# Performance work log

Hardware: AMD Instinct MI355X
Metric: run time of the kernel (lower is better)

The kernel has to match this reference:

```python
import jax, jax.numpy as jnp
import numpy as np

B, S, D = 2, 2048, 2048
H, KV, HD = 16, 8, 128
THETA = 1000000.0
EPS = 1e-6


def rms_norm(x, w, eps=EPS):
    # normalize over last dim (head_dim), per Qwen3 q_norm/k_norm
    var = jnp.mean(jnp.square(x), axis=-1, keepdims=True)
    return x * jax.lax.rsqrt(var + eps) * w


def rope_cos_sin(seq_len, head_dim, theta=THETA, dtype=jnp.float32):
    inv_freq = 1.0 / (theta ** (jnp.arange(0, head_dim, 2, dtype=jnp.float32) / head_dim))
    pos = jnp.arange(seq_len, dtype=jnp.float32)
    freqs = jnp.outer(pos, inv_freq)              # [S, HD/2]
    emb = jnp.concatenate([freqs, freqs], axis=-1)  # [S, HD]
    return jnp.cos(emb).astype(dtype), jnp.sin(emb).astype(dtype)


def rotate_half(x):
    x1, x2 = jnp.split(x, 2, axis=-1)
    return jnp.concatenate([-x2, x1], axis=-1)


def setup_inputs() -> dict:
    key = jax.random.key(0)
    ks = jax.random.split(key, 8)
    sd = 1.0 / np.sqrt(D)
    return {
        "x": jax.random.normal(ks[0], (B, S, D), jnp.float32),
        "attention_mask": jnp.zeros((B, 1, S, S), jnp.float32),
        "wq": jax.random.normal(ks[1], (H * HD, D), jnp.float32) * sd,
        "wk": jax.random.normal(ks[2], (KV * HD, D), jnp.float32) * sd,
        "wv": jax.random.normal(ks[3], (KV * HD, D), jnp.float32) * sd,
        "wo": jax.random.normal(ks[4], (D, H * HD), jnp.float32) * sd,
        "q_norm_w": jnp.ones((HD,), jnp.float32),
        "k_norm_w": jnp.ones((HD,), jnp.float32),
    }


def reference(x, attention_mask, wq, wk, wv, wo, q_norm_w, k_norm_w):
    b, s, d = x.shape
    # QKV projections
    q = (x @ wq.T).reshape(b, s, H, HD)
    k = (x @ wk.T).reshape(b, s, KV, HD)
    v = (x @ wv.T).reshape(b, s, KV, HD)
    # Qwen3 per-head RMSNorm on q and k
    q = rms_norm(q, q_norm_w)
    k = rms_norm(k, k_norm_w)
    # RoPE
    cos, sin = rope_cos_sin(s, HD, dtype=x.dtype)
    cos = cos[None, :, None, :]
    sin = sin[None, :, None, :]
    q = q * cos + rotate_half(q) * sin
    k = k * cos + rotate_half(k) * sin
    # GQA: repeat kv heads to H query heads
    rep = H // KV
    k = jnp.repeat(k, rep, axis=2)  # [b, s, H, HD]
    v = jnp.repeat(v, rep, axis=2)
    # attention
    scale = 1.0 / np.sqrt(HD)
    logits = jnp.einsum("bqhd,bkhd->bhqk", q, k) * scale
    logits = logits + attention_mask
    causal = jnp.tril(jnp.ones((s, s), bool))
    logits = jnp.where(causal[None, None], logits, jnp.asarray(-1e9, logits.dtype))
    probs = jax.nn.softmax(logits, axis=-1)
    out = jnp.einsum("bhqk,bkhd->bqhd", probs, v).reshape(b, s, H * HD)
    return out @ wo.T
```

## Files before the change

kernel.cpp:

```cpp
#include <hip/hip_runtime.h>
#include <hip/hip_bf16.h>

typedef unsigned short u16;
typedef __attribute__((ext_vector_type(8))) short s16x8;
typedef __attribute__((ext_vector_type(4))) float f32x4;

#define NB 2
#define SQ 2048
#define DM 2048
#define NH 16
#define NKV 8
#define HD 128

__device__ __forceinline__ float bf2f(u16 u) {
    return __uint_as_float(((unsigned)u) << 16);
}
__device__ __forceinline__ u16 f2bf(float f) {
    unsigned u = __float_as_uint(f);
    u += 0x7FFFu + ((u >> 16) & 1u);
    return (u16)(u >> 16);
}

__device__ __forceinline__ void gload16(const void* g, void* l) {
    __builtin_amdgcn_global_load_lds((__attribute__((address_space(1))) void*)g,
                                     (__attribute__((address_space(3))) void*)l,
                                     16, 0, 0);
}

#define X4   2097152u
#define WQ4  1048576u
#define WK4   524288u
#define WV4   524288u
#define WO4  1048576u
#define P0 X4
#define P1 (P0 + WQ4)
#define P2 (P1 + WK4)
#define P3 (P2 + WV4)
#define P4 (P3 + WO4)

__global__ __launch_bounds__(256) void cvt5(const float* __restrict__ x,
                                            const float* __restrict__ wq,
                                            const float* __restrict__ wk,
                                            const float* __restrict__ wv,
                                            const float* __restrict__ wo,
                                            u16* __restrict__ xb, u16* __restrict__ wqb,
                                            u16* __restrict__ wkb, u16* __restrict__ wvb,
                                            u16* __restrict__ wob) {
    unsigned i4 = blockIdx.x * 256u + threadIdx.x;
    if (i4 >= P4) return;
    const float* src; u16* dst; unsigned off;
    if (i4 < P0)      { src = x;  dst = xb;  off = i4; }
    else if (i4 < P1) { src = wq; dst = wqb; off = i4 - P0; }
    else if (i4 < P2) { src = wk; dst = wkb; off = i4 - P1; }
    else if (i4 < P3) { src = wv; dst = wvb; off = i4 - P2; }
    else              { src = wo; dst = wob; off = i4 - P3; }
    float4 v = ((const float4*)src)[off];
    ushort4 o;
    o.x = f2bf(v.x); o.y = f2bf(v.y); o.z = f2bf(v.z); o.w = f2bf(v.w);
    ((ushort4*)dst)[off] = o;
}

__global__ __launch_bounds__(512) void gemm_qkv(const u16* __restrict__ A,
                                                const u16* __restrict__ wqb,
                                                const u16* __restrict__ wkb,
                                                const u16* __restrict__ wvb,
                                                u16* __restrict__ q_ws,
                                                u16* __restrict__ k_ws,
                                                u16* __restrict__ vt_ws) {
    __shared__ u16 SA[2][2][256 * 32];
    __shared__ u16 SB[2][2][256 * 32];
    const int K = DM;
    const int t_ = threadIdx.x;
    const int w = t_ >> 6, lane = t_ & 63;
    const int lr = lane & 15, lg = lane >> 4;
    const int bid = blockIdx.x;
    const int swz = (bid & 7) * 32 + (bid >> 3);
    const int m0 = (swz >> 4) * 256, n0 = (swz & 15) * 256;
    const int wr = w >> 2, wc = w & 3;

    const u16* W; int nloc;
    if (n0 < 2048)      { W = wqb; nloc = n0; }
    else if (n0 < 3072) { W = wkb; nloc = n0 - 2048; }
    else                { W = wvb; nloc = n0 - 3072; }

    const int srow = t_ >> 2;
    const int sc4 = t_ & 3;
    const int schk = (sc4 ^ ((srow >> 1) & 3)) * 8;

#define STG_A(ks, bufq, kk)                                                      \
    {                                                                            \
        gload16(&A[(size_t)(m0 + srow) * K + (kk) + (ks)*32 + schk],             \
                &SA[bufq][ks][(w * 16) * 32]);                                   \
        gload16(&A[(size_t)(m0 + 128 + srow) * K + (kk) + (ks)*32 + schk],       \
                &SA[bufq][ks][(128 + w * 16) * 32]);                             \
    }
#define STG_B(ks, bufq, kk)                                                      \
    {                                                                            \
        gload16(&W[(size_t)(nloc + srow) * K + (kk) + (ks)*32 + schk],           \
                &SB[bufq][ks][(w * 16) * 32]);                                   \
        gload16(&W[(size_t)(nloc + 128 + srow) * K + (kk) + (ks)*32 + schk],     \
                &SB[bufq][ks][(128 + w * 16) * 32]);                             \
    }

    f32x4 acc[8][4];
#pragma unroll
    for (int i = 0; i < 8; ++i)
#pragma unroll
        for (int j = 0; j < 4; ++j) acc[i][j] = (f32x4){0.f, 0.f, 0.f, 0.f};

    const int rchk = (lg ^ ((lr >> 1) & 3)) * 8;

    STG_A(0, 0, 0); STG_B(0, 0, 0); STG_A(1, 0, 0); STG_B(1, 0, 0);
    asm volatile("s_waitcnt vmcnt(4)\n\ts_barrier" ::: "memory");

    const int NT = K / 64;
    for (int t = 0; t < NT; ++t) {
        const int pb = t & 1, nbuf = pb ^ 1;
        const int kk = (t + 1) * 64;
        const bool more = (t < NT - 1);

        s16x8 af[4], bf[4];

        if (more) STG_A(0, nbuf, kk);
#pragma unroll
        for (int fc = 0; fc < 4; ++fc)
            bf[fc] = *(const s16x8*)&SB[pb][0][(wc * 64 + fc * 16 + lr) * 32 + rchk];
#pragma unroll
        for (int fi = 0; fi < 4; ++fi)
            af[fi] = *(const s16x8*)&SA[pb][0][(wr * 128 + fi * 16 + lr) * 32 + rchk];
        __builtin_amdgcn_s_setprio(1);
#pragma unroll
        for (int fi = 0; fi < 4; ++fi)
#pragma unroll
            for (int fc = 0; fc < 4; ++fc)
                acc[fi][fc] = __builtin_amdgcn_mfma_f32_16x16x32_bf16(
                    af[fi], bf[fc], acc[fi][fc], 0, 0, 0);
        __builtin_amdgcn_s_setprio(0);

        if (more) STG_B(0, nbuf, kk);
#pragma unroll
        for (int fi = 0; fi < 4; ++fi)
            af[fi] = *(const s16x8*)&SA[pb][0][(wr * 128 + 64 + fi * 16 + lr) * 32 + rchk];
        __builtin_amdgcn_s_setprio(1);
#pragma unroll
        for (int fi = 0; fi < 4; ++fi)
#pragma unroll
            for (int fc = 0; fc < 4; ++fc)
                acc[4 + fi][fc] = __builtin_amdgcn_mfma_f32_16x16x32_bf16(
                    af[fi], bf[fc], acc[4 + fi][fc], 0, 0, 0);
        __builtin_amdgcn_s_setprio(0);

        if (more) asm volatile("s_waitcnt vmcnt(4)\n\ts_barrier" ::: "memory");
        else      asm volatile("s_waitcnt vmcnt(0)\n\ts_barrier" ::: "memory");

        if (more) STG_A(1, nbuf, kk);
#pragma unroll
        for (int fc = 0; fc < 4; ++fc)
            bf[fc] = *(const s16x8*)&SB[pb][1][(wc * 64 + fc * 16 + lr) * 32 + rchk];
#pragma unroll
        for (int fi = 0; fi < 4; ++fi)
            af[fi] = *(const s16x8*)&SA[pb][1][(wr * 128 + fi * 16 + lr) * 32 + rchk];
        __builtin_amdgcn_s_setprio(1);
#pragma unroll
        for (int fi = 0; fi < 4; ++fi)
#pragma unroll
            for (int fc = 0; fc < 4; ++fc)
                acc[fi][fc] = __builtin_amdgcn_mfma_f32_16x16x32_bf16(
                    af[fi], bf[fc], acc[fi][fc], 0, 0, 0);
        __builtin_amdgcn_s_setprio(0);

        if (more) STG_B(1, nbuf, kk);
#pragma unroll
        for (int fi = 0; fi < 4; ++fi)
            af[fi] = *(const s16x8*)&SA[pb][1][(wr * 128 + 64 + fi * 16 + lr) * 32 + rchk];
        __builtin_amdgcn_s_setprio(1);
#pragma unroll
        for (int fi = 0; fi < 4; ++fi)
#pragma unroll
            for (int fc = 0; fc < 4; ++fc)
                acc[4 + fi][fc] = __builtin_amdgcn_mfma_f32_16x16x32_bf16(
                    af[fi], bf[fc], acc[4 + fi][fc], 0, 0, 0);
        __builtin_amdgcn_s_setprio(0);

        if (more) asm volatile("s_waitcnt vmcnt(4)\n\ts_barrier" ::: "memory");
    }
#undef STG_A
#undef STG_B

#pragma unroll
    for (int fr = 0; fr < 8; ++fr)
#pragma unroll
        for (int fc = 0; fc < 4; ++fc)
#pragma unroll
            for (int j = 0; j < 4; ++j) {
                int m = m0 + wr * 128 + fr * 16 + lg * 4 + j;
                int n = n0 + wc * 64 + fc * 16 + lr;
                u16 v = f2bf(acc[fr][fc][j]);
                if (n0 < 2048) {
                    q_ws[(size_t)m * 2048 + n] = v;
                } else if (n0 < 3072) {
                    k_ws[(size_t)m * 1024 + (n - 2048)] = v;
                } else {
                    int b = m >> 11, sl = m & 2047;
                    vt_ws[((size_t)b * 1024 + (n - 3072)) * 2048 + sl] = v;
                }
            }
}

__global__ __launch_bounds__(256) void gemm_out(const u16* __restrict__ A,
                                                const u16* __restrict__ W,
                                                float* __restrict__ C,
                                                int M, int N, int K) {
    __shared__ u16 Alds[128 * 32];
    __shared__ u16 Blds[128 * 32];
    const int t = threadIdx.x;
    const int w = t >> 6, lane = t & 63;
    const int lr = lane & 15, lg = lane >> 4;
    const int m0 = blockIdx.y * 128, n0 = blockIdx.x * 128;
    const int wr = w >> 1, wc = w & 1;

    f32x4 acc[4][4];
#pragma unroll
    for (int i = 0; i < 4; ++i)
#pragma unroll
        for (int j = 0; j < 4; ++j) acc[i][j] = (f32x4){0.f, 0.f, 0.f, 0.f};

    const int r_a = lane >> 2;
    const int c_a = (lane & 3) * 8;

    for (int k0 = 0; k0 < K; k0 += 32) {
#pragma unroll
        for (int s = 0; s < 2; ++s) {
            int chunk = s * 4 + w;
            int row = chunk * 16 + r_a;
            gload16(&A[(size_t)(m0 + row) * K + k0 + c_a], &Alds[chunk * 512]);
            gload16(&W[(size_t)(n0 + row) * K + k0 + c_a], &Blds[chunk * 512]);
        }
        asm volatile("s_waitcnt vmcnt(0)" ::: "memory");
        __syncthreads();

        s16x8 af[4], bfr[4];
#pragma unroll
        for (int mi = 0; mi < 4; ++mi)
            af[mi] = *(const s16x8*)&Alds[(wr * 64 + mi * 16 + lr) * 32 + lg * 8];
#pragma unroll
        for (int ni = 0; ni < 4; ++ni)
            bfr[ni] = *(const s16x8*)&Blds[(wc * 64 + ni * 16 + lr) * 32 + lg * 8];
#pragma unroll
        for (int mi = 0; mi < 4; ++mi)
#pragma unroll
            for (int ni = 0; ni < 4; ++ni)
                acc[mi][ni] = __builtin_amdgcn_mfma_f32_16x16x32_bf16(
                    af[mi], bfr[ni], acc[mi][ni], 0, 0, 0);
        __syncthreads();
    }

#pragma unroll
    for (int mi = 0; mi < 4; ++mi)
#pragma unroll
        for (int ni = 0; ni < 4; ++ni)
#pragma unroll
            for (int j = 0; j < 4; ++j) {
                int m = m0 + wr * 64 + mi * 16 + lg * 4 + j;
                int n = n0 + wc * 64 + ni * 16 + lr;
                C[(size_t)m * N + n] = acc[mi][ni][j];
            }
}

__global__ __launch_bounds__(256) void rmsrope(u16* __restrict__ qb, u16* __restrict__ kb,
                                               const float* __restrict__ qw,
                                               const float* __restrict__ kw) {
    int wid = blockIdx.x * 4 + (threadIdx.x >> 6);
    int lane = threadIdx.x & 63;
    u16* base;
    const float* w;
    int pos;
    float sc;
    if (wid < NB * SQ * NH) {
        int h = wid & (NH - 1), tok = wid >> 4;
        pos = tok & (SQ - 1);
        base = qb + ((size_t)tok * NH + h) * HD;
        w = qw;
        sc = 0.08838834764831845f;
    } else {
        int f = wid - NB * SQ * NH;
        int h = f & (NKV - 1), tok = f >> 3;
        pos = tok & (SQ - 1);
        base = kb + ((size_t)tok * NKV + h) * HD;
        w = kw;
        sc = 1.0f;
    }
    float x1 = bf2f(base[lane]), x2 = bf2f(base[lane + 64]);
    float ss = x1 * x1 + x2 * x2;
#pragma unroll
    for (int off = 32; off; off >>= 1) ss += __shfl_xor(ss, off);
    float r = rsqrtf(ss * (1.f / 128.f) + 1e-6f);
    x1 *= r * w[lane];
    x2 *= r * w[lane + 64];
    float inv = exp2f((float)lane * (-19.931568569324174f / 64.f));
    float fr = (float)pos * inv;
    float c = cosf(fr);
    float sn = sinf(fr);
    base[lane]      = f2bf(sc * (x1 * c - x2 * sn));
    base[lane + 64] = f2bf(sc * (x2 * c + x1 * sn));
}

__global__ __launch_bounds__(256) void flash(const u16* __restrict__ q,
                                             const u16* __restrict__ k,
                                             const u16* __restrict__ vt,
                                             u16* __restrict__ o) {
    __shared__ u16 KB[64][128];
    __shared__ u16 VB[128][64];
    __shared__ u16 plds[4][16][72];
    const int id = blockIdx.x;
    const int i_ = id >> 3;
    const int g = (id & 7) * 2 + (i_ >> 5);
    const int kvh = g >> 1, b = g & 1;
    const int j_ = i_ & 31;
    const int h = kvh * 2 + (j_ >> 4);
    const int bx = j_ & 15;
    const int t = threadIdx.x;
    const int w = t >> 6, lane = t & 63;
    const int lr = lane & 15, lg = lane >> 4;

    const u16* kbase = k + (size_t)(b * SQ) * 1024 + kvh * 128;
    const u16* vbase = vt + (size_t)(b * NKV + kvh) * HD * SQ;

    for (int sidx = 0; sidx < 2; ++sidx) {
        const int qt = sidx ? (31 - bx) : bx;
        const int qrow = qt * 64 + w * 16;

        s16x8 qf[4];
        const size_t qbase = ((size_t)(b * SQ + qrow + lr) * NH + h) * HD;
#pragma unroll
        for (int ds = 0; ds < 4; ++ds)
            qf[ds] = *(const s16x8*)&q[qbase + ds * 32 + lg * 8];

        f32x4 oacc[8];
#pragma unroll
        for (int dt = 0; dt < 8; ++dt) oacc[dt] = (f32x4){0.f, 0.f, 0.f, 0.f};
        float mrow[4] = {-1e30f, -1e30f, -1e30f, -1e30f};
        float lrow[4] = {0.f, 0.f, 0.f, 0.f};

#pragma unroll
        for (int i = 0; i < 4; ++i) {
            int qq = i * 256 + t;
            int r = qq >> 4, c = qq & 15;
            gload16(kbase + (size_t)r * 1024 + (c ^ (r & 7)) * 8,
                    &KB[0][0] + i * 2048 + w * 512);
        }
        __syncthreads();

        for (int kt = 0; kt <= qt; ++kt) {
            const int kv0 = kt * 64;
#pragma unroll
            for (int i = 0; i < 4; ++i) {
                int qq = i * 256 + t;
                int r = qq >> 3, c = qq & 7;
                gload16(vbase + (size_t)r * SQ + kv0 + (c ^ (r & 7)) * 8,
                        &VB[0][0] + i * 2048 + w * 512);
            }

            f32x4 sc[4];
#pragma unroll
            for (int ct = 0; ct < 4; ++ct) sc[ct] = (f32x4){0.f, 0.f, 0.f, 0.f};
#pragma unroll
            for (int ds = 0; ds < 4; ++ds) {
                s16x8 kf[4];
#pragma unroll
                for (int ct = 0; ct < 4; ++ct)
                    kf[ct] = *(const s16x8*)&KB[ct * 16 + lr][((ds * 4 + lg) ^ (lr & 7)) * 8];
                __builtin_amdgcn_s_setprio(1);
#pragma unroll
                for (int ct = 0; ct < 4; ++ct)
                    sc[ct] = __builtin_amdgcn_mfma_f32_16x16x32_bf16(qf[ds], kf[ct], sc[ct], 0, 0, 0);
                __builtin_amdgcn_s_setprio(0);
            }
            if (kt == qt) {
#pragma unroll
                for (int ct = 0; ct < 4; ++ct)
#pragma unroll
                    for (int j = 0; j < 4; ++j)
                        if ((kv0 + ct * 16 + lr) > (qrow + lg * 4 + j))
                            sc[ct][j] = -1e30f;
            }
            float mnew[4], sfac[4];
#pragma unroll
            for (int j = 0; j < 4; ++j) {
                float tm = fmaxf(fmaxf(sc[0][j], sc[1][j]), fmaxf(sc[2][j], sc[3][j]));
#pragma unroll
                for (int off = 1; off < 16; off <<= 1) tm = fmaxf(tm, __shfl_xor(tm, off));
                mnew[j] = fmaxf(mrow[j], tm);
                sfac[j] = __expf(mrow[j] - mnew[j]);
                mrow[j] = mnew[j];
            }
#pragma unroll
            for (int ct = 0; ct < 4; ++ct)
#pragma unroll
                for (int j = 0; j < 4; ++j) sc[ct][j] = __expf(sc[ct][j] - mnew[j]);
#pragma unroll
            for (int j = 0; j < 4; ++j) {
                float ssum = sc[0][j] + sc[1][j] + sc[2][j] + sc[3][j];
#pragma unroll
                for (int off = 1; off < 16; off <<= 1) ssum += __shfl_xor(ssum, off);
                lrow[j] = lrow[j] * sfac[j] + ssum;
            }
#pragma unroll
            for (int dt = 0; dt < 8; ++dt)
#pragma unroll
                for (int j = 0; j < 4; ++j) oacc[dt][j] *= sfac[j];

#pragma unroll
            for (int ct = 0; ct < 4; ++ct)
#pragma unroll
                for (int j = 0; j < 4; ++j)
                    plds[w][lg * 4 + j][ct * 16 + lr] = f2bf(sc[ct][j]);
            s16x8 pf0 = *(const s16x8*)&plds[w][lr][lg * 8];
            s16x8 pf1 = *(const s16x8*)&plds[w][lr][32 + lg * 8];

            __syncthreads();

            if (kt < qt) {
#pragma unroll
                for (int i = 0; i < 4; ++i) {
                    int qq = i * 256 + t;
                    int r = qq >> 4, c = qq & 15;
                    gload16(kbase + (size_t)(kv0 + 64 + r) * 1024 + (c ^ (r & 7)) * 8,
                            &KB[0][0] + i * 2048 + w * 512);
                }
            }

#pragma unroll
            for (int dt = 0; dt < 8; ++dt) {
                s16x8 vf0 = *(const s16x8*)&VB[dt * 16 + lr][(lg ^ (lr & 7)) * 8];
                s16x8 vf1 = *(const s16x8*)&VB[dt * 16 + lr][((4 + lg) ^ (lr & 7)) * 8];
                __builtin_amdgcn_s_setprio(1);
                oacc[dt] = __builtin_amdgcn_mfma_f32_16x16x32_bf16(pf0, vf0, oacc[dt], 0, 0, 0);
                oacc[dt] = __builtin_amdgcn_mfma_f32_16x16x32_bf16(pf1, vf1, oacc[dt], 0, 0, 0);
                __builtin_amdgcn_s_setprio(0);
            }
            __syncthreads();
        }

        float inv_l[4];
#pragma unroll
        for (int j = 0; j < 4; ++j) inv_l[j] = 1.f / lrow[j];
#pragma unroll
        for (int dt = 0; dt < 8; ++dt)
#pragma unroll
            for (int j = 0; j < 4; ++j) {
                int tok = b * SQ + qrow + lg * 4 + j;
                o[((size_t)tok * NH + h) * HD + dt * 16 + lr] = f2bf(oacc[dt][j] * inv_l[j]);
            }
    }
}

extern "C" void kernel_launch(void* const* d_in, const int* in_sizes, int n_in,
                              void* d_out, int out_size, void* d_ws, size_t ws_size,
                              hipStream_t stream) {
    (void)in_sizes; (void)n_in; (void)out_size; (void)ws_size;
    const float* x   = (const float*)d_in[0];
    const float* wq  = (const float*)d_in[2];
    const float* wk  = (const float*)d_in[3];
    const float* wv  = (const float*)d_in[4];
    const float* wo  = (const float*)d_in[5];
    const float* qnw = (const float*)d_in[6];
    const float* knw = (const float*)d_in[7];

    u16* xb    = (u16*)d_ws;
    u16* q_ws  = xb    + (size_t)4096 * 2048;
    u16* k_ws  = q_ws  + (size_t)4096 * 2048;
    u16* vt_ws = k_ws  + (size_t)4096 * 1024;
    u16* wqb   = vt_ws + (size_t)4096 * 1024;
    u16* wkb   = wqb   + (size_t)2048 * 2048;
    u16* wvb   = wkb   + (size_t)1024 * 2048;
    u16* wob   = wvb   + (size_t)1024 * 2048;

    const int M = NB * SQ;

    cvt5<<<(P4 + 255) / 256, 256, 0, stream>>>(x, wq, wk, wv, wo, xb, wqb, wkb, wvb, wob);

    gemm_qkv<<<256, 512, 0, stream>>>(xb, wqb, wkb, wvb, q_ws, k_ws, vt_ws);

    rmsrope<<<(NB * SQ * (NH + NKV)) / 4, 256, 0, stream>>>(q_ws, k_ws, qnw, knw);

    flash<<<512, 256, 0, stream>>>(q_ws, k_ws, vt_ws, q_ws);

    gemm_out<<<dim3(DM / 128, M / 128), 256, 0, stream>>>(q_ws, wob, (float*)d_out, M, DM, DM);
}
```

Before: 279.9 us.

## Use three-stage LDS ring buffer with one barrier per k-slice in QKV GEMM

The QKV projection GEMM moves from a double-buffered pair of 64-wide k-tiles to a three-slot ring of 32-wide k-slices. Each iteration waits on one barrier and prefetches two slices ahead. This cuts LDS use from 64KB to 48KB and keeps more loads in flight. In exchange it doubles the number of loop iterations and barriers per k extent, and the per-barrier MFMA work is smaller.

Measured after the change: 286.4 us. +2.3%, slower.

```diff
diff --git a/kernel.cpp b/kernel.cpp
--- a/kernel.cpp
+++ b/kernel.cpp
@@ -67,8 +67,8 @@
                                                 u16* __restrict__ q_ws,
                                                 u16* __restrict__ k_ws,
                                                 u16* __restrict__ vt_ws) {
-    __shared__ u16 SA[2][2][256 * 32];
-    __shared__ u16 SB[2][2][256 * 32];
+    __shared__ u16 SA[3][256 * 32];
+    __shared__ u16 SB[3][256 * 32];
     const int K = DM;
     const int t_ = threadIdx.x;
     const int w = t_ >> 6, lane = t_ & 63;
@@ -87,20 +87,19 @@
     const int sc4 = t_ & 3;
     const int schk = (sc4 ^ ((srow >> 1) & 3)) * 8;
 
-#define STG_A(ks, bufq, kk)                                                      \
+#define STG(tt)                                                                  \
     {                                                                            \
-        gload16(&A[(size_t)(m0 + srow) * K + (kk) + (ks)*32 + schk],             \
-                &SA[bufq][ks][(w * 16) * 32]);                                   \
-        gload16(&A[(size_t)(m0 + 128 + srow) * K + (kk) + (ks)*32 + schk],       \
-                &SA[bufq][ks][(128 + w * 16) * 32]);                             \
+        const int kb_ = (tt) * 32;                                               \
+        const int bq_ = (tt) % 3;                                                \
+        gload16(&A[(size_t)(m0 + srow) * K + kb_ + schk],                        \
+                &SA[bq_][(w * 16) * 32]);                                        \
+        gload16(&A[(size_t)(m0 + 128 + srow) * K + kb_ + schk],                  \
+                &SA[bq_][(128 + w * 16) * 32]);                                  \
+        gload16(&W[(size_t)(nloc + srow) * K + kb_ + schk],                      \
+                &SB[bq_][(w * 16) * 32]);                                        \
+        gload16(&W[(size_t)(nloc + 128 + srow) * K + kb_ + schk],                \
+                &SB[bq_][(128 + w * 16) * 32]);                                  \
     }
-#define STG_B(ks, bufq, kk)                                                      \
-    {                                                                            \
-        gload16(&W[(size_t)(nloc + srow) * K + (kk) + (ks)*32 + schk],           \
-                &SB[bufq][ks][(w * 16) * 32]);                                   \
-        gload16(&W[(size_t)(nloc + 128 + srow) * K + (kk) + (ks)*32 + schk],     \
-                &SB[bufq][ks][(128 + w * 16) * 32]);                             \
-    }
 
     f32x4 acc[8][4];
 #pragma unroll
@@ -110,24 +109,24 @@
 
     const int rchk = (lg ^ ((lr >> 1) & 3)) * 8;
 
-    STG_A(0, 0, 0); STG_B(0, 0, 0); STG_A(1, 0, 0); STG_B(1, 0, 0);
-    asm volatile("s_waitcnt vmcnt(4)\n\ts_barrier" ::: "memory");
-
-    const int NT = K / 64;
+    STG(0); STG(1);
+
+    const int NT = K / 32;
     for (int t = 0; t < NT; ++t) {
-        const int pb = t & 1, nbuf = pb ^ 1;
-        const int kk = (t + 1) * 64;
-        const bool more = (t < NT - 1);
-
+        if (t < NT - 1) asm volatile("s_waitcnt vmcnt(4)\n\ts_barrier" ::: "memory");
+        else            asm volatile("s_waitcnt vmcnt(0)\n\ts_barrier" ::: "memory");
+        if (t + 2 < NT) STG(t + 2);
+
+        const u16* pA = &SA[t % 3][0];
+        const u16* pB = &SB[t % 3][0];
         s16x8 af[4], bf[4];
-
-        if (more) STG_A(0, nbuf, kk);
 #pragma unroll
         for (int fc = 0; fc < 4; ++fc)
-            bf[fc] = *(const s16x8*)&SB[pb][0][(wc * 64 + fc * 16 + lr) * 32 + rchk];
+            bf[fc] = *(const s16x8*)&pB[(wc * 64 + fc * 16 + lr) * 32 + rchk];
+
 #pragma unroll
         for (int fi = 0; fi < 4; ++fi)
-            af[fi] = *(const s16x8*)&SA[pb][0][(wr * 128 + fi * 16 + lr) * 32 + rchk];
+            af[fi] = *(const s16x8*)&pA[(wr * 128 + fi * 16 + lr) * 32 + rchk];
         __builtin_amdgcn_s_setprio(1);
 #pragma unroll
         for (int fi = 0; fi < 4; ++fi)
@@ -137,10 +136,9 @@
                     af[fi], bf[fc], acc[fi][fc], 0, 0, 0);
         __builtin_amdgcn_s_setprio(0);
 
-        if (more) STG_B(0, nbuf, kk);
 #pragma unroll
         for (int fi = 0; fi < 4; ++fi)
-            af[fi] = *(const s16x8*)&SA[pb][0][(wr * 128 + 64 + fi * 16 + lr) * 32 + rchk];
+            af[fi] = *(const s16x8*)&pA[(wr * 128 + 64 + fi * 16 + lr) * 32 + rchk];
         __builtin_amdgcn_s_setprio(1);
 #pragma unroll
         for (int fi = 0; fi < 4; ++fi)
@@ -149,43 +147,8 @@
                 acc[4 + fi][fc] = __builtin_amdgcn_mfma_f32_16x16x32_bf16(
                     af[fi], bf[fc], acc[4 + fi][fc], 0, 0, 0);
         __builtin_amdgcn_s_setprio(0);
-
-        if (more) asm volatile("s_waitcnt vmcnt(4)\n\ts_barrier" ::: "memory");
-        else      asm volatile("s_waitcnt vmcnt(0)\n\ts_barrier" ::: "memory");
-
-        if (more) STG_A(1, nbuf, kk);
-#pragma unroll
-        for (int fc = 0; fc < 4; ++fc)
-            bf[fc] = *(const s16x8*)&SB[pb][1][(wc * 64 + fc * 16 + lr) * 32 + rchk];
-#pragma unroll
-        for (int fi = 0; fi < 4; ++fi)
-            af[fi] = *(const s16x8*)&SA[pb][1][(wr * 128 + fi * 16 + lr) * 32 + rchk];
-        __builtin_amdgcn_s_setprio(1);
-#pragma unroll
-        for (int fi = 0; fi < 4; ++fi)
-#pragma unroll
-            for (int fc = 0; fc < 4; ++fc)
-                acc[fi][fc] = __builtin_amdgcn_mfma_f32_16x16x32_bf16(
-                    af[fi], bf[fc], acc[fi][fc], 0, 0, 0);
-        __builtin_amdgcn_s_setprio(0);
-
-        if (more) STG_B(1, nbuf, kk);
-#pragma unroll
-        for (int fi = 0; fi < 4; ++fi)
-            af[fi] = *(const s16x8*)&SA[pb][1][(wr * 128 + 64 + fi * 16 + lr) * 32 + rchk];
-        __builtin_amdgcn_s_setprio(1);
-#pragma unroll
-        for (int fi = 0; fi < 4; ++fi)
-#pragma unroll
-            for (int fc = 0; fc < 4; ++fc)
-                acc[4 + fi][fc] = __builtin_amdgcn_mfma_f32_16x16x32_bf16(
-                    af[fi], bf[fc], acc[4 + fi][fc], 0, 0, 0);
-        __builtin_amdgcn_s_setprio(0);
-
-        if (more) asm volatile("s_waitcnt vmcnt(4)\n\ts_barrier" ::: "memory");
     }
-#undef STG_A
-#undef STG_B
+#undef STG
 
 #pragma unroll
     for (int fr = 0; fr < 8; ++fr)
```

## Rewrite output GEMM with 256x256 tiles, double-buffered LDS, swizzle

Applied to the files above, without the earlier changes.

Replaces the simple 128x128 output-projection GEMM with a 512-thread 256x256-tile kernel. It double-buffers 64-wide K slices in LDS and overlaps the next tile's global-to-LDS loads with MFMA work. It also XOR-swizzles LDS chunks to reduce bank conflicts, remaps block indices for L2 locality, and raises wave priority around the MFMA bursts. Only 128 blocks launch, which may leave some of the chip's many CUs idle, and the larger register and LDS footprint lowers occupancy.

Result: slower. 290.8 us (+3.9%).

```diff
diff --git a/kernel.cpp b/kernel.cpp
--- a/kernel.cpp
+++ b/kernel.cpp
@@ -207,63 +207,133 @@
             }
 }
 
-__global__ __launch_bounds__(256) void gemm_out(const u16* __restrict__ A,
+__global__ __launch_bounds__(512) void gemm_out(const u16* __restrict__ A,
                                                 const u16* __restrict__ W,
-                                                float* __restrict__ C,
-                                                int M, int N, int K) {
-    __shared__ u16 Alds[128 * 32];
-    __shared__ u16 Blds[128 * 32];
-    const int t = threadIdx.x;
-    const int w = t >> 6, lane = t & 63;
+                                                float* __restrict__ C) {
+    __shared__ u16 SA[2][2][256 * 32];
+    __shared__ u16 SB[2][2][256 * 32];
+    const int K = DM;
+    const int t_ = threadIdx.x;
+    const int w = t_ >> 6, lane = t_ & 63;
     const int lr = lane & 15, lg = lane >> 4;
-    const int m0 = blockIdx.y * 128, n0 = blockIdx.x * 128;
-    const int wr = w >> 1, wc = w & 1;
-
-    f32x4 acc[4][4];
-#pragma unroll
-    for (int i = 0; i < 4; ++i)
+    const int bid = blockIdx.x;
+    const int swz = (bid & 7) * 16 + (bid >> 3);
+    const int m0 = (swz >> 3) * 256, n0 = (swz & 7) * 256;
+    const int wr = w >> 2, wc = w & 3;
+
+    const int srow = t_ >> 2;
+    const int sc4 = t_ & 3;
+    const int schk = (sc4 ^ ((srow >> 1) & 3)) * 8;
+
+#define STG_A(ks, bufq, kk)                                                      \
+    {                                                                            \
+        gload16(&A[(size_t)(m0 + srow) * K + (kk) + (ks)*32 + schk],             \
+                &SA[bufq][ks][(w * 16) * 32]);                                   \
+        gload16(&A[(size_t)(m0 + 128 + srow) * K + (kk) + (ks)*32 + schk],       \
+                &SA[bufq][ks][(128 + w * 16) * 32]);                             \
+    }
+#define STG_B(ks, bufq, kk)                                                      \
+    {                                                                            \
+        gload16(&W[(size_t)(n0 + srow) * K + (kk) + (ks)*32 + schk],             \
+                &SB[bufq][ks][(w * 16) * 32]);                                   \
+        gload16(&W[(size_t)(n0 + 128 + srow) * K + (kk) + (ks)*32 + schk],       \
+                &SB[bufq][ks][(128 + w * 16) * 32]);                             \
+    }
+
+    f32x4 acc[8][4];
+#pragma unroll
+    for (int i = 0; i < 8; ++i)
 #pragma unroll
         for (int j = 0; j < 4; ++j) acc[i][j] = (f32x4){0.f, 0.f, 0.f, 0.f};
 
-    const int r_a = lane >> 2;
-    const int c_a = (lane & 3) * 8;
-
-    for (int k0 = 0; k0 < K; k0 += 32) {
-#pragma unroll
-        for (int s = 0; s < 2; ++s) {
-            int chunk = s * 4 + w;
-            int row = chunk * 16 + r_a;
-            gload16(&A[(size_t)(m0 + row) * K + k0 + c_a], &Alds[chunk * 512]);
-            gload16(&W[(size_t)(n0 + row) * K + k0 + c_a], &Blds[chunk * 512]);
-        }
-        asm volatile("s_waitcnt vmcnt(0)" ::: "memory");
-        __syncthreads();
-
-        s16x8 af[4], bfr[4];
-#pragma unroll
-        for (int mi = 0; mi < 4; ++mi)
-            af[mi] = *(const s16x8*)&Alds[(wr * 64 + mi * 16 + lr) * 32 + lg * 8];
-#pragma unroll
-        for (int ni = 0; ni < 4; ++ni)
-            bfr[ni] = *(const s16x8*)&Blds[(wc * 64 + ni * 16 + lr) * 32 + lg * 8];
-#pragma unroll
-        for (int mi = 0; mi < 4; ++mi)
-#pragma unroll
-            for (int ni = 0; ni < 4; ++ni)
-                acc[mi][ni] = __builtin_amdgcn_mfma_f32_16x16x32_bf16(
-                    af[mi], bfr[ni], acc[mi][ni], 0, 0, 0);
-        __syncthreads();
-    }
-
-#pragma unroll
-    for (int mi = 0; mi < 4; ++mi)
-#pragma unroll
-        for (int ni = 0; ni < 4; ++ni)
+    const int rchk = (lg ^ ((lr >> 1) & 3)) * 8;
+
+    STG_A(0, 0, 0); STG_B(0, 0, 0); STG_A(1, 0, 0); STG_B(1, 0, 0);
+    asm volatile("s_waitcnt vmcnt(4)\n\ts_barrier" ::: "memory");
+
+    const int NT = K / 64;
+    for (int t = 0; t < NT; ++t) {
+        const int pb = t & 1, nbuf = pb ^ 1;
+        const int kk = (t + 1) * 64;
+        const bool more = (t < NT - 1);
+
+        s16x8 af[4], bf[4];
+
+        if (more) STG_A(0, nbuf, kk);
+#pragma unroll
+        for (int fc = 0; fc < 4; ++fc)
+            bf[fc] = *(const s16x8*)&SB[pb][0][(wc * 64 + fc * 16 + lr) * 32 + rchk];
+#pragma unroll
+        for (int fi = 0; fi < 4; ++fi)
+            af[fi] = *(const s16x8*)&SA[pb][0][(wr * 128 + fi * 16 + lr) * 32 + rchk];
+        __builtin_amdgcn_s_setprio(1);
+#pragma unroll
+        for (int fi = 0; fi < 4; ++fi)
+#pragma unroll
+            for (int fc = 0; fc < 4; ++fc)
+                acc[fi][fc] = __builtin_amdgcn_mfma_f32_16x16x32_bf16(
+                    af[fi], bf[fc], acc[fi][fc], 0, 0, 0);
+        __builtin_amdgcn_s_setprio(0);
+
+        if (more) STG_B(0, nbuf, kk);
+#pragma unroll
+        for (int fi = 0; fi < 4; ++fi)
+            af[fi] = *(const s16x8*)&SA[pb][0][(wr * 128 + 64 + fi * 16 + lr) * 32 + rchk];
+        __builtin_amdgcn_s_setprio(1);
+#pragma unroll
+        for (int fi = 0; fi < 4; ++fi)
+#pragma unroll
+            for (int fc = 0; fc < 4; ++fc)
+                acc[4 + fi][fc] = __builtin_amdgcn_mfma_f32_16x16x32_bf16(
+                    af[fi], bf[fc], acc[4 + fi][fc], 0, 0, 0);
+        __builtin_amdgcn_s_setprio(0);
+
+        if (more) asm volatile("s_waitcnt vmcnt(4)\n\ts_barrier" ::: "memory");
+        else      asm volatile("s_waitcnt vmcnt(0)\n\ts_barrier" ::: "memory");
+
+        if (more) STG_A(1, nbuf, kk);
+#pragma unroll
+        for (int fc = 0; fc < 4; ++fc)
+            bf[fc] = *(const s16x8*)&SB[pb][1][(wc * 64 + fc * 16 + lr) * 32 + rchk];
+#pragma unroll
+        for (int fi = 0; fi < 4; ++fi)
+            af[fi] = *(const s16x8*)&SA[pb][1][(wr * 128 + fi * 16 + lr) * 32 + rchk];
+        __builtin_amdgcn_s_setprio(1);
+#pragma unroll
+        for (int fi = 0; fi < 4; ++fi)
+#pragma unroll
+            for (int fc = 0; fc < 4; ++fc)
+                acc[fi][fc] = __builtin_amdgcn_mfma_f32_16x16x32_bf16(
+                    af[fi], bf[fc], acc[fi][fc], 0, 0, 0);
+        __builtin_amdgcn_s_setprio(0);
+
+        if (more) STG_B(1, nbuf, kk);
+#pragma unroll
+        for (int fi = 0; fi < 4; ++fi)
+            af[fi] = *(const s16x8*)&SA[pb][1][(wr * 128 + 64 + fi * 16 + lr) * 32 + rchk];
+        __builtin_amdgcn_s_setprio(1);
+#pragma unroll
+        for (int fi = 0; fi < 4; ++fi)
+#pragma unroll
+            for (int fc = 0; fc < 4; ++fc)
+                acc[4 + fi][fc] = __builtin_amdgcn_mfma_f32_16x16x32_bf16(
+                    af[fi], bf[fc], acc[4 + fi][fc], 0, 0, 0);
+        __builtin_amdgcn_s_setprio(0);
+
+        if (more) asm volatile("s_waitcnt vmcnt(4)\n\ts_barrier" ::: "memory");
+    }
+#undef STG_A
+#undef STG_B
+
+#pragma unroll
+    for (int fr = 0; fr < 8; ++fr)
+#pragma unroll
+        for (int fc = 0; fc < 4; ++fc)
 #pragma unroll
             for (int j = 0; j < 4; ++j) {
-                int m = m0 + wr * 64 + mi * 16 + lg * 4 + j;
-                int n = n0 + wc * 64 + ni * 16 + lr;
-                C[(size_t)m * N + n] = acc[mi][ni][j];
+                int m = m0 + wr * 128 + fr * 16 + lg * 4 + j;
+                int n = n0 + wc * 64 + fc * 16 + lr;
+                C[(size_t)m * 2048 + n] = acc[fr][fc][j];
             }
 }
 
@@ -486,5 +556,5 @@
 
     flash<<<512, 256, 0, stream>>>(q_ws, k_ws, vt_ws, q_ws);
 
-    gemm_out<<<dim3(DM / 128, M / 128), 256, 0, stream>>>(q_ws, wob, (float*)d_out, M, DM, DM);
-}
+    gemm_out<<<128, 512, 0, stream>>>(q_ws, wob, (float*)d_out);
+}
```
